# Optimization experiments

Measured on AMD Instinct MI355X. Metric: run time of the kernel, lower is better.

Reference implementation:

```python
import jax, jax.numpy as jnp
import numpy as np

ACT_BITS = 8
Q_B = 2 ** (ACT_BITS - 1)          # 128
EPS = 1e-6                          # module epsilon
GN_EPS = 1e-5                       # torch GroupNorm default eps
SCALE = 0.01                        # fixed ternary weight scale (buffer)
STRIDE = 1
PADDING = 1


def setup_inputs() -> dict:
    key = jax.random.key(0)
    k1, k2 = jax.random.split(key)
    x = jax.random.normal(k1, (16, 256, 64, 64), dtype=jnp.float32)
    weight = jax.random.normal(k2, (256, 256, 3, 3), dtype=jnp.float32)
    bias = jnp.zeros((256,), dtype=jnp.float32)
    ln_weight = jnp.ones((256,), dtype=jnp.float32)
    ln_bias = jnp.zeros((256,), dtype=jnp.float32)
    return {"x": x, "weight": weight, "bias": bias,
            "ln_weight": ln_weight, "ln_bias": ln_bias}


def _group_norm_1group(x, gamma, beta):
    # GroupNorm(1, C): normalize over (C, H, W) per sample, per-channel affine.
    mean = jnp.mean(x, axis=(1, 2, 3), keepdims=True)
    var = jnp.var(x, axis=(1, 2, 3), keepdims=True)
    xn = (x - mean) * jax.lax.rsqrt(var + GN_EPS)
    return xn * gamma[None, :, None, None] + beta[None, :, None, None]


def reference(x, weight, bias, ln_weight, ln_bias):
    # 1) GroupNorm
    x_ln = _group_norm_1group(x, ln_weight, ln_bias)

    # 2) BitNet absmax activation quantization (global absmax)
    gamma = jnp.maximum(jnp.max(jnp.abs(x_ln)), EPS)
    x_scaled = x_ln * (Q_B / gamma)
    x_clipped = jnp.clip(x_scaled, -Q_B + EPS, Q_B - EPS)
    x_quant = jnp.round(x_clipped)

    # 3) Ternary weight quantization with fixed scale: {-SCALE, 0, +SCALE}
    delta = 0.7 * jnp.mean(jnp.abs(weight))  # TTQ threshold
    w_q = jnp.where(weight > delta, SCALE,
                    jnp.where(weight < -delta, -SCALE, 0.0)).astype(weight.dtype)

    # 4) Conv2d (NCHW, OIHW)
    y = jax.lax.conv_general_dilated(
        x_quant, w_q,
        window_strides=(STRIDE, STRIDE),
        padding=[(PADDING, PADDING), (PADDING, PADDING)],
        dimension_numbers=("NCHW", "OIHW", "NCHW"),
        feature_group_count=1,
    )

    # 5) Dequant + bias
    y = y * (gamma / Q_B) + bias[None, :, None, None]
    return y
```

## Files before the change

### kernel.cpp

```cpp
#include <hip/hip_runtime.h>
#include <hip/hip_bf16.h>

#define CHW   1048576
#define XQ_BYTES 35684352u
#define WQ_OFF   35684352u
#define GNP_OFF  36864000u
#define CMM_OFF  36880384u
#define MR_OFF   36913152u
#define SC_OFF   36913280u
#define WP_OFF   36913296u
#define DL_OFF   36913584u

typedef __attribute__((ext_vector_type(8)))  short short8;
typedef __attribute__((ext_vector_type(16))) float f32x16;

__device__ __forceinline__ unsigned short f2bf(float f) {
    __hip_bfloat16 h = __float2bfloat16(f);
    return __builtin_bit_cast(unsigned short, h);
}

__device__ __forceinline__ void gload16(const void* g, void* l) {
    __builtin_amdgcn_global_load_lds(
        (const __attribute__((address_space(1))) unsigned int*)(unsigned long long)(g),
        (__attribute__((address_space(3))) unsigned int*)(unsigned int)(unsigned long long)(l),
        16, 0, 0);
}

__global__ void k_pass1(const float* __restrict__ x, double2* __restrict__ part,
                        float2* __restrict__ cmm) {
    int bid = blockIdx.x;
    int n = bid >> 6, c4 = bid & 63;
    int t = threadIdx.x, ch = t >> 6, lane = t & 63;
    int c = c4 * 4 + ch;
    const float4* p = (const float4*)(x + (size_t)n * CHW + (size_t)c * 4096);
    double s = 0.0, ss = 0.0;
    float mn = 1e30f, mx = -1e30f;
#pragma unroll
    for (int k = 0; k < 16; ++k) {
        float4 v = p[k * 64 + lane];
        mn = fminf(mn, fminf(fminf(v.x, v.y), fminf(v.z, v.w)));
        mx = fmaxf(mx, fmaxf(fmaxf(v.x, v.y), fmaxf(v.z, v.w)));
        double dx = v.x, dy = v.y, dz = v.z, dw = v.w;
        s  += dx + dy + dz + dw;
        ss += dx * dx + dy * dy + dz * dz + dw * dw;
    }
    for (int o = 32; o; o >>= 1) {
        s += __shfl_down(s, o); ss += __shfl_down(ss, o);
        mn = fminf(mn, __shfl_down(mn, o)); mx = fmaxf(mx, __shfl_down(mx, o));
    }
    __shared__ double sh0[4], sh1[4];
    if (lane == 0) {
        cmm[n * 256 + c] = make_float2(mn, mx);
        sh0[ch] = s; sh1[ch] = ss;
    }
    __syncthreads();
    if (t == 0)
        part[bid] = make_double2(sh0[0] + sh0[1] + sh0[2] + sh0[3],
                                 sh1[0] + sh1[1] + sh1[2] + sh1[3]);
}

__global__ void k_wsum(const float* __restrict__ w, double* __restrict__ wp) {
    int blk = blockIdx.x, t = threadIdx.x;
    const float4* p = (const float4*)(w + (size_t)blk * 16384);
    double s = 0.0;
#pragma unroll
    for (int j = 0; j < 16; ++j) {
        float4 v = p[j * 256 + t];
        s += fabs((double)v.x) + fabs((double)v.y) + fabs((double)v.z) + fabs((double)v.w);
    }
    for (int o = 32; o; o >>= 1) s += __shfl_down(s, o);
    __shared__ double sh[4];
    if ((t & 63) == 0) sh[t >> 6] = s;
    __syncthreads();
    if (t == 0) wp[blk] = sh[0] + sh[1] + sh[2] + sh[3];
}

__global__ void k_scalars(const double2* __restrict__ part, const float2* __restrict__ cmm,
                          const float* __restrict__ lnw, const float* __restrict__ lnb,
                          const double* __restrict__ wp,
                          float2* __restrict__ mr, float* __restrict__ sc,
                          float* __restrict__ dl) {
    __shared__ float shm[16], shr[16];
    int t = threadIdx.x;
    {
        int n = t >> 4, i = t & 15;
        double s = 0.0, ss = 0.0;
#pragma unroll
        for (int k = 0; k < 4; ++k) {
            double2 v = part[n * 64 + i * 4 + k];
            s += v.x; ss += v.y;
        }
        for (int o = 8; o; o >>= 1) { s += __shfl_down(s, o); ss += __shfl_down(ss, o); }
        if (i == 0) {
            double mean = s * (1.0 / 1048576.0);
            double var  = ss * (1.0 / 1048576.0) - mean * mean;
            shm[n] = (float)mean; shr[n] = (float)(1.0 / sqrt(var + 1e-5));
        }
    }
    __syncthreads();
    if (t < 16) mr[t] = make_float2(shm[t], shr[t]);
    float m = 0.0f;
#pragma unroll
    for (int k = 0; k < 16; ++k) {
        int idx = t + k * 256;
        int n = idx >> 8, c = idx & 255;
        float2 v = cmm[idx];
        float scale = lnw[c] * shr[n];
        float shift = lnb[c] - shm[n] * scale;
        m = fmaxf(m, fmaxf(fabsf(v.x * scale + shift), fabsf(v.y * scale + shift)));
    }
    for (int o = 32; o; o >>= 1) m = fmaxf(m, __shfl_down(m, o));
    __shared__ float shg[4];
    if ((t & 63) == 0) shg[t >> 6] = m;
    __syncthreads();
    if (t == 0) {
        float gamma = fmaxf(fmaxf(fmaxf(shg[0], shg[1]), fmaxf(shg[2], shg[3])), 1e-6f);
        sc[0] = gamma;
        sc[1] = 128.0f / gamma;
        sc[2] = (gamma / 128.0f) * 0.01f;
    }
    if (t < 64) {
        double s = (t < 36) ? wp[t] : 0.0;
        for (int o = 32; o; o >>= 1) s += __shfl_down(s, o);
        if (t == 0) dl[0] = (float)(0.7 * (s / 589824.0));
    }
}

__global__ void k_wquant(const float* __restrict__ w, const float* __restrict__ dl,
                         unsigned short* __restrict__ wq) {
    __shared__ float sw[2304];
    int co = blockIdx.x, t = threadIdx.x;
    const float* wr = w + (size_t)co * 2304;
#pragma unroll
    for (int j = 0; j < 9; ++j) sw[j * 256 + t] = wr[j * 256 + t];
    __syncthreads();
    float d = dl[0];
#pragma unroll
    for (int tap = 0; tap < 9; ++tap) {
        float v = sw[t * 9 + tap];
        float s = (v > d) ? 1.0f : ((v < -d) ? -1.0f : 0.0f);
        wq[tap * 65536 + co * 256 + t] = f2bf(s);
    }
}

__global__ void k_halo(unsigned short* __restrict__ xq) {
    int idx = blockIdx.x * 8 + (threadIdx.x >> 5);
    int n = idx / 260, p = idx - n * 260;
    int hh, ww;
    if (p < 66)       { hh = 0;        ww = p; }
    else if (p < 132) { hh = 65;       ww = p - 66; }
    else if (p < 196) { hh = p - 131;  ww = 0; }
    else              { hh = p - 195;  ww = 65; }
    uint4 z = make_uint4(0, 0, 0, 0);
    *(uint4*)(xq + ((size_t)(n * 66 + hh) * 66 + ww) * 256 + (threadIdx.x & 31) * 8) = z;
}

__global__ void k_quantx(const float* __restrict__ x, const float2* __restrict__ mr,
                         const float* __restrict__ sc, const float* __restrict__ lnw,
                         const float* __restrict__ lnb, unsigned short* __restrict__ xq) {
    int bid = blockIdx.x;
    int n = bid >> 6, hg = (bid >> 2) & 15, cg = bid & 3;
    int t = threadIdx.x;
    int w = t & 63, h = hg * 4 + (t >> 6);
    float2 m = mr[n];
    float s128 = sc[1];
    uint q[32];
    const float* xp = x + (((size_t)n * 256 + cg * 64) * 64 + h) * 64 + w;
#pragma unroll
    for (int ci = 0; ci < 64; ++ci) {
        int c = cg * 64 + ci;
        float g = lnw[c] * m.y;
        float be = lnb[c];
        float v = xp[(size_t)ci * 4096];
        float xs = ((v - m.x) * g + be) * s128;
        xs = fminf(fmaxf(xs, -(128.0f - 1e-6f)), (128.0f - 1e-6f));
        unsigned short ub = f2bf(rintf(xs));
        if (ci & 1) q[ci >> 1] |= ((uint)ub << 16);
        else        q[ci >> 1]  = ub;
    }
    unsigned short* op = xq + ((size_t)(n * 66 + h + 1) * 66 + (w + 1)) * 256 + cg * 64;
    uint4* o4 = (uint4*)op;
#pragma unroll
    for (int s2 = 0; s2 < 8; ++s2)
        o4[s2] = make_uint4(q[s2 * 4], q[s2 * 4 + 1], q[s2 * 4 + 2], q[s2 * 4 + 3]);
}

#define ATRI  16384
#define BBASE 49152
#define BBUF  16384

#define LD8(off) (*(const short8*)&lds[(off)])

#define STAGE_B(BS) { \
    const int _so = BBASE + (BS) * BBUF + dAB; \
    gload16(bSrc + stB,        &lds[_so]); \
    gload16(bSrc + stB + 2048, &lds[_so + 512]); \
    gload16(bSrc + stB + 4096, &lds[_so + 1024]); \
    gload16(bSrc + stB + 6144, &lds[_so + 1536]); \
    if (bKc < 3) { bKc++; stB += 64; } else { bKc = 0; stB += 65344; } }

#define STAGE_A(AS) { \
    const int _so = (AS) * ATRI + dAB; \
    gload16(aSrc + stA,        &lds[_so]); \
    gload16(aSrc + stA + 2048, &lds[_so + 512]); \
    gload16(aSrc + stA + 4096, &lds[_so + 1024]); \
    gload16(aSrc + stA + 6144, &lds[_so + 1536]); \
    if (aKc < 3) { aKc++; stA += 64; } \
    else { aKc = 0; if (aTx < 2) { aTx++; stA += 64; } else { aTx = 0; stA += 16192; } } }

#define ITER(AR, BR, AS, BS, DOA, DOB, W) { \
    const int _abo = (AR) * ATRI; \
    const int _bbo = BBASE + (BR) * BBUF; \
    if (DOB) STAGE_B(BS) \
    if (DOA) STAGE_A(AS) \
    short8 b00 = LD8(_bbo + rB0 + sp0), b01 = LD8(_bbo + rB0 + sp1); \
    short8 b02 = LD8(_bbo + rB0 + sp2), b03 = LD8(_bbo + rB0 + sp3); \
    short8 b10 = LD8(_bbo + rB1 + sp0), b11 = LD8(_bbo + rB1 + sp1); \
    short8 b12 = LD8(_bbo + rB1 + sp2), b13 = LD8(_bbo + rB1 + sp3); \
    _Pragma("unroll") \
    for (int _m = 0; _m < 4; ++_m) { \
        const int _ra = _abo + rA0 + _m * 2048; \
        short8 a0 = LD8(_ra + sp0), a1 = LD8(_ra + sp1); \
        short8 a2 = LD8(_ra + sp2), a3 = LD8(_ra + sp3); \
        __builtin_amdgcn_s_setprio(1); \
        acc[_m][0] = __builtin_amdgcn_mfma_f32_32x32x16_bf16(a0, b00, acc[_m][0], 0, 0, 0); \
        acc[_m][1] = __builtin_amdgcn_mfma_f32_32x32x16_bf16(a0, b10, acc[_m][1], 0, 0, 0); \
        acc[_m][0] = __builtin_amdgcn_mfma_f32_32x32x16_bf16(a1, b01, acc[_m][0], 0, 0, 0); \
        acc[_m][1] = __builtin_amdgcn_mfma_f32_32x32x16_bf16(a1, b11, acc[_m][1], 0, 0, 0); \
        acc[_m][0] = __builtin_amdgcn_mfma_f32_32x32x16_bf16(a2, b02, acc[_m][0], 0, 0, 0); \
        acc[_m][1] = __builtin_amdgcn_mfma_f32_32x32x16_bf16(a2, b12, acc[_m][1], 0, 0, 0); \
        acc[_m][0] = __builtin_amdgcn_mfma_f32_32x32x16_bf16(a3, b03, acc[_m][0], 0, 0, 0); \
        acc[_m][1] = __builtin_amdgcn_mfma_f32_32x32x16_bf16(a3, b13, acc[_m][1], 0, 0, 0); \
        __builtin_amdgcn_s_setprio(0); \
    } \
    if ((W) == 4)      { asm volatile("s_waitcnt vmcnt(4)" ::: "memory"); } \
    else if ((W) == 0) { asm volatile("s_waitcnt vmcnt(0)" ::: "memory"); } \
    __builtin_amdgcn_s_barrier(); \
    __builtin_amdgcn_sched_barrier(0); \
}

#define STORE4(P, A, BV) { \
    float4 v0; v0.x = (A)[0]*qs+(BV);  v0.y = (A)[1]*qs+(BV);  v0.z = (A)[2]*qs+(BV);  v0.w = (A)[3]*qs+(BV);  *(float4*)((P))      = v0; \
    float4 v1; v1.x = (A)[4]*qs+(BV);  v1.y = (A)[5]*qs+(BV);  v1.z = (A)[6]*qs+(BV);  v1.w = (A)[7]*qs+(BV);  *(float4*)((P) + 8)  = v1; \
    float4 v2; v2.x = (A)[8]*qs+(BV);  v2.y = (A)[9]*qs+(BV);  v2.z = (A)[10]*qs+(BV); v2.w = (A)[11]*qs+(BV); *(float4*)((P) + 16) = v2; \
    float4 v3; v3.x = (A)[12]*qs+(BV); v3.y = (A)[13]*qs+(BV); v3.z = (A)[14]*qs+(BV); v3.w = (A)[15]*qs+(BV); *(float4*)((P) + 24) = v3; }

__global__ __launch_bounds__(512, 2) void k_conv(const unsigned short* __restrict__ xq,
                                                 const unsigned short* __restrict__ wq,
                                                 const float* __restrict__ sc,
                                                 const float* __restrict__ bias,
                                                 float* __restrict__ out) {
    __shared__ unsigned short lds[81920];
    int t = threadIdx.x, wv = t >> 6, l = t & 63;
    int wm = wv >> 2, wn = wv & 3;
    int l31 = l & 31, l5 = l >> 5;

    int bid = ((int)blockIdx.x & 7) * 32 + ((int)blockIdx.x >> 3);
    int n = bid >> 4, h2 = (bid & 15) << 2;

    int rowg = l >> 3;
    int lg   = (l & 7) ^ rowg;
    const unsigned short* aSrc = xq +
        ((size_t)((n * 66 + h2 + (wv >> 1)) * 66 + (wv & 1) * 32 + rowg)) * 256 + lg * 8;
    const unsigned short* bSrc = wq + (size_t)(wv * 32 + rowg) * 256 + lg * 8;
    const int dAB = wv * 2048;

    int q7  = l31 & 7;
    int sp0 = ((0 + l5) ^ q7) * 8;
    int sp1 = ((2 + l5) ^ q7) * 8;
    int sp2 = ((4 + l5) ^ q7) * 8;
    int sp3 = ((6 + l5) ^ q7) * 8;
    int rA0 = (wm * 128 + l31) * 64;
    int rB0 = (wn * 64 + l31) * 64;
    int rB1 = rB0 + 2048;

    f32x16 acc[4][2] = {};

    gload16(aSrc,        &lds[dAB]);
    gload16(aSrc + 2048, &lds[dAB + 512]);
    gload16(aSrc + 4096, &lds[dAB + 1024]);
    gload16(aSrc + 6144, &lds[dAB + 1536]);
    gload16(bSrc,        &lds[BBASE + dAB]);
    gload16(bSrc + 2048, &lds[BBASE + dAB + 512]);
    gload16(bSrc + 4096, &lds[BBASE + dAB + 1024]);
    gload16(bSrc + 6144, &lds[BBASE + dAB + 1536]);
    gload16(aSrc + 64,        &lds[ATRI + dAB]);
    gload16(aSrc + 64 + 2048, &lds[ATRI + dAB + 512]);
    gload16(aSrc + 64 + 4096, &lds[ATRI + dAB + 1024]);
    gload16(aSrc + 64 + 6144, &lds[ATRI + dAB + 1536]);
    asm volatile("s_waitcnt vmcnt(4)" ::: "memory");
    __builtin_amdgcn_s_barrier();
    __builtin_amdgcn_sched_barrier(0);

    int stA = 128, aKc = 2, aTx = 0;
    int stB = 64,  bKc = 1;

#pragma unroll 1
    for (int it = 0; it < 5; ++it) {
        ITER(0, 0, 2, 1, 1, 1, 4)
        ITER(1, 1, 0, 0, 1, 1, 4)
        ITER(2, 0, 1, 1, 1, 1, 4)
        ITER(0, 1, 2, 0, 1, 1, 4)
        ITER(1, 0, 0, 1, 1, 1, 4)
        ITER(2, 1, 1, 0, 1, 1, 4)
    }
    ITER(0, 0, 2, 1, 1, 1, 4)
    ITER(1, 1, 0, 0, 1, 1, 4)
    ITER(2, 0, 1, 1, 1, 1, 4)
    ITER(0, 1, 2, 0, 1, 1, 4)
    ITER(1, 0, 0, 1, 0, 1, 0)
    ITER(2, 1, 0, 0, 0, 0, -1)

    float qs = sc[2];
#pragma unroll
    for (int m = 0; m < 4; ++m) {
        int h = h2 + wm * 2 + (m >> 1);
        int wb = (m & 1) * 32 + l5 * 4;
        size_t obase = (size_t)n * CHW + (size_t)h * 64 + wb;
#pragma unroll
        for (int nf = 0; nf < 2; ++nf) {
            int co = wn * 64 + nf * 32 + l31;
            float bv = bias[co];
            float* ob = out + obase + (size_t)co * 4096;
            STORE4(ob, acc[m][nf], bv)
        }
    }
}

extern "C" void kernel_launch(void* const* d_in, const int* in_sizes, int n_in,
                              void* d_out, int out_size, void* d_ws, size_t ws_size,
                              hipStream_t stream) {
    (void)in_sizes; (void)n_in; (void)out_size; (void)ws_size;
    const float* x    = (const float*)d_in[0];
    const float* wgt  = (const float*)d_in[1];
    const float* bias = (const float*)d_in[2];
    const float* lnw  = (const float*)d_in[3];
    const float* lnb  = (const float*)d_in[4];
    float* out = (float*)d_out;
    char* ws = (char*)d_ws;

    unsigned short* xq = (unsigned short*)ws;
    unsigned short* wq = (unsigned short*)(ws + WQ_OFF);
    double2* gnp = (double2*)(ws + GNP_OFF);
    float2*  cmm = (float2*)(ws + CMM_OFF);
    float2*  mr  = (float2*)(ws + MR_OFF);
    float*   sc  = (float*)(ws + SC_OFF);
    double*  wp  = (double*)(ws + WP_OFF);
    float*   dl  = (float*)(ws + DL_OFF);

    k_pass1  <<<1024, 256, 0, stream>>>(x, gnp, cmm);
    k_wsum   <<<36,   256, 0, stream>>>(wgt, wp);
    k_scalars<<<1,    256, 0, stream>>>(gnp, cmm, lnw, lnb, wp, mr, sc, dl);
    k_wquant <<<256,  256, 0, stream>>>(wgt, dl, wq);
    k_halo   <<<520,  256, 0, stream>>>(xq);
    k_quantx <<<1024, 256, 0, stream>>>(x, mr, sc, lnw, lnb, xq);
    k_conv   <<<256,  512, 0, stream>>>(xq, wq, sc, bias, out);
}
```

Before: 121.5 us.

## Switch conv to int8 MFMA with overflow-fixup pass for +128 activations

Quantized activations and ternary weights are stored as int8 instead of bf16, and the conv uses i32 32x32x32 int8 MFMA, which halves operand bytes and doubles K per instruction. Because +128 does not fit in int8, such values are clamped to 127 and recorded in an event list, and a separate fixup kernel atomically adds the missing contribution to the output. The quantx kernel is also re-tiled to a different thread and block mapping. The fixup path relies on a capped list of 1024 events and adds atomics and an extra launch.

```diff
diff --git a/kernel.cpp b/kernel.cpp
--- a/kernel.cpp
+++ b/kernel.cpp
@@ -2,22 +2,19 @@
 #include <hip/hip_bf16.h>
 
 #define CHW   1048576
-#define XQ_BYTES 35684352u
-#define WQ_OFF   35684352u
-#define GNP_OFF  36864000u
-#define CMM_OFF  36880384u
-#define MR_OFF   36913152u
-#define SC_OFF   36913280u
-#define WP_OFF   36913296u
-#define DL_OFF   36913584u
-
-typedef __attribute__((ext_vector_type(8)))  short short8;
-typedef __attribute__((ext_vector_type(16))) float f32x16;
-
-__device__ __forceinline__ unsigned short f2bf(float f) {
-    __hip_bfloat16 h = __float2bfloat16(f);
-    return __builtin_bit_cast(unsigned short, h);
-}
+#define XQ_BYTES 17842176u
+#define WQ_OFF   17842176u
+#define GNP_OFF  18432000u
+#define CMM_OFF  18448384u
+#define MR_OFF   18481152u
+#define SC_OFF   18481280u
+#define WP_OFF   18481296u
+#define DL_OFF   18481584u
+#define EVC_OFF  18481588u
+#define EVL_OFF  18481592u
+
+typedef __attribute__((ext_vector_type(4)))  int i32x4;
+typedef __attribute__((ext_vector_type(16))) int i32x16;
 
 __device__ __forceinline__ void gload16(const void* g, void* l) {
     __builtin_amdgcn_global_load_lds(
@@ -79,7 +76,7 @@
                           const float* __restrict__ lnw, const float* __restrict__ lnb,
                           const double* __restrict__ wp,
                           float2* __restrict__ mr, float* __restrict__ sc,
-                          float* __restrict__ dl) {
+                          float* __restrict__ dl, int* __restrict__ evcnt) {
     __shared__ float shm[16], shr[16];
     int t = threadIdx.x;
     {
@@ -99,6 +96,7 @@
     }
     __syncthreads();
     if (t < 16) mr[t] = make_float2(shm[t], shr[t]);
+    if (t == 0) evcnt[0] = 0;
     float m = 0.0f;
 #pragma unroll
     for (int k = 0; k < 16; ++k) {
@@ -127,7 +125,7 @@
 }
 
 __global__ void k_wquant(const float* __restrict__ w, const float* __restrict__ dl,
-                         unsigned short* __restrict__ wq) {
+                         signed char* __restrict__ wq) {
     __shared__ float sw[2304];
     int co = blockIdx.x, t = threadIdx.x;
     const float* wr = w + (size_t)co * 2304;
@@ -138,12 +136,12 @@
 #pragma unroll
     for (int tap = 0; tap < 9; ++tap) {
         float v = sw[t * 9 + tap];
-        float s = (v > d) ? 1.0f : ((v < -d) ? -1.0f : 0.0f);
-        wq[tap * 65536 + co * 256 + t] = f2bf(s);
-    }
-}
-
-__global__ void k_halo(unsigned short* __restrict__ xq) {
+        int s = (v > d) ? 1 : ((v < -d) ? -1 : 0);
+        wq[tap * 65536 + co * 256 + t] = (signed char)s;
+    }
+}
+
+__global__ void k_halo(unsigned char* __restrict__ xq) {
     int idx = blockIdx.x * 8 + (threadIdx.x >> 5);
     int n = idx / 260, p = idx - n * 260;
     int hh, ww;
@@ -151,106 +149,122 @@
     else if (p < 132) { hh = 65;       ww = p - 66; }
     else if (p < 196) { hh = p - 131;  ww = 0; }
     else              { hh = p - 195;  ww = 65; }
-    uint4 z = make_uint4(0, 0, 0, 0);
-    *(uint4*)(xq + ((size_t)(n * 66 + hh) * 66 + ww) * 256 + (threadIdx.x & 31) * 8) = z;
+    *(uint2*)(xq + ((size_t)(n * 66 + hh) * 66 + ww) * 256 + (threadIdx.x & 31) * 8) =
+        make_uint2(0, 0);
 }
 
 __global__ void k_quantx(const float* __restrict__ x, const float2* __restrict__ mr,
                          const float* __restrict__ sc, const float* __restrict__ lnw,
-                         const float* __restrict__ lnb, unsigned short* __restrict__ xq) {
+                         const float* __restrict__ lnb, unsigned char* __restrict__ xq,
+                         int* __restrict__ evcnt, int* __restrict__ evlist) {
     int bid = blockIdx.x;
-    int n = bid >> 6, hg = (bid >> 2) & 15, cg = bid & 3;
+    int n = bid >> 8, r = bid & 255;
+    int h = r >> 2, wg = r & 3;
     int t = threadIdx.x;
-    int w = t & 63, h = hg * 4 + (t >> 6);
+    int g = t & 15, p = t >> 4;
+    int w = wg * 16 + p;
     float2 m = mr[n];
     float s128 = sc[1];
-    uint q[32];
-    const float* xp = x + (((size_t)n * 256 + cg * 64) * 64 + h) * 64 + w;
-#pragma unroll
-    for (int ci = 0; ci < 64; ++ci) {
-        int c = cg * 64 + ci;
-        float g = lnw[c] * m.y;
-        float be = lnb[c];
-        float v = xp[(size_t)ci * 4096];
-        float xs = ((v - m.x) * g + be) * s128;
-        xs = fminf(fmaxf(xs, -(128.0f - 1e-6f)), (128.0f - 1e-6f));
-        unsigned short ub = f2bf(rintf(xs));
-        if (ci & 1) q[ci >> 1] |= ((uint)ub << 16);
-        else        q[ci >> 1]  = ub;
-    }
-    unsigned short* op = xq + ((size_t)(n * 66 + h + 1) * 66 + (w + 1)) * 256 + cg * 64;
-    uint4* o4 = (uint4*)op;
-#pragma unroll
-    for (int s2 = 0; s2 < 8; ++s2)
-        o4[s2] = make_uint4(q[s2 * 4], q[s2 * 4 + 1], q[s2 * 4 + 2], q[s2 * 4 + 3]);
-}
-
-#define ATRI  16384
+    const float* xp = x + ((size_t)n * 256 + g * 16) * 4096 + h * 64 + w;
+    uint u[4];
+#pragma unroll
+    for (int j = 0; j < 16; ++j) {
+        int c = g * 16 + j;
+        float gg = lnw[c] * m.y, be = lnb[c];
+        float v = xp[(size_t)j * 4096];
+        float xs = ((v - m.x) * gg + be) * s128;
+        xs = fminf(fmaxf(xs, -(128.0f - 1e-6f)), 128.0f - 1e-6f);
+        int q = (int)rintf(xs);
+        if (q == 128) {
+            int idx = atomicAdd(evcnt, 1);
+            if (idx < 1024) evlist[idx] = (n << 20) | (h << 14) | (w << 8) | c;
+            q = 127;
+        }
+        uint b = (uint)(q & 255);
+        if ((j & 3) == 0) u[j >> 2] = b; else u[j >> 2] |= b << ((j & 3) * 8);
+    }
+    *(uint4*)(xq + ((size_t)((n * 66 + h + 1) * 66) + (w + 1)) * 256 + g * 16) =
+        make_uint4(u[0], u[1], u[2], u[3]);
+}
+
+__global__ void k_fix(const signed char* __restrict__ wq, const int* __restrict__ evcnt,
+                      const int* __restrict__ evlist, const float* __restrict__ sc,
+                      float* __restrict__ out) {
+    int cnt = *evcnt; if (cnt > 1024) cnt = 1024;
+    float qs = sc[2];
+    int co = threadIdx.x;
+    for (int e = blockIdx.x; e < cnt; e += gridDim.x) {
+        int pk = evlist[e];
+        int n = pk >> 20, h = (pk >> 14) & 63, w = (pk >> 8) & 63, ci = pk & 255;
+#pragma unroll
+        for (int ty = 0; ty < 3; ++ty)
+#pragma unroll
+            for (int tx = 0; tx < 3; ++tx) {
+                int i = h + 1 - ty, j = w + 1 - tx;
+                if (i < 0 || i > 63 || j < 0 || j > 63) continue;
+                int sgn = wq[(ty * 3 + tx) * 65536 + co * 256 + ci];
+                if (sgn)
+                    atomicAdd(out + (((size_t)n * 256 + co) * 64 + i) * 64 + j,
+                              qs * (float)sgn);
+            }
+    }
+}
+
+#define ABUF  16384
 #define BBASE 49152
-#define BBUF  16384
-
-#define LD8(off) (*(const short8*)&lds[(off)])
-
-#define STAGE_B(BS) { \
-    const int _so = BBASE + (BS) * BBUF + dAB; \
-    gload16(bSrc + stB,        &lds[_so]); \
-    gload16(bSrc + stB + 2048, &lds[_so + 512]); \
-    gload16(bSrc + stB + 4096, &lds[_so + 1024]); \
-    gload16(bSrc + stB + 6144, &lds[_so + 1536]); \
-    if (bKc < 3) { bKc++; stB += 64; } else { bKc = 0; stB += 65344; } }
+#define LD16(off) (*(const i32x4*)&lds8[(off)])
+#define MFMA_I8(A, B, C) __builtin_amdgcn_mfma_i32_32x32x32_i8(A, B, C, 0, 0, 0)
 
 #define STAGE_A(AS) { \
-    const int _so = (AS) * ATRI + dAB; \
-    gload16(aSrc + stA,        &lds[_so]); \
-    gload16(aSrc + stA + 2048, &lds[_so + 512]); \
-    gload16(aSrc + stA + 4096, &lds[_so + 1024]); \
-    gload16(aSrc + stA + 6144, &lds[_so + 1536]); \
+    const int _so = (AS) * ABUF + wv * 1024; \
+    gload16(aSrc + stA,         lds8 + _so); \
+    gload16(aSrc + stA + 33792, lds8 + _so + 8192); \
     if (aKc < 3) { aKc++; stA += 64; } \
     else { aKc = 0; if (aTx < 2) { aTx++; stA += 64; } else { aTx = 0; stA += 16192; } } }
 
+#define STAGE_B(BS) { \
+    const int _so = BBASE + (BS) * ABUF + wv * 1024; \
+    gload16(bSrc + stB,         lds8 + _so); \
+    gload16(bSrc + stB + 32768, lds8 + _so + 8192); \
+    if (bKc < 3) { bKc++; stB += 64; } else { bKc = 0; stB += 65344; } }
+
 #define ITER(AR, BR, AS, BS, DOA, DOB, W) { \
-    const int _abo = (AR) * ATRI; \
-    const int _bbo = BBASE + (BR) * BBUF; \
+    const int _ab = (AR) * ABUF; \
+    const int _bb = BBASE + (BR) * ABUF; \
     if (DOB) STAGE_B(BS) \
     if (DOA) STAGE_A(AS) \
-    short8 b00 = LD8(_bbo + rB0 + sp0), b01 = LD8(_bbo + rB0 + sp1); \
-    short8 b02 = LD8(_bbo + rB0 + sp2), b03 = LD8(_bbo + rB0 + sp3); \
-    short8 b10 = LD8(_bbo + rB1 + sp0), b11 = LD8(_bbo + rB1 + sp1); \
-    short8 b12 = LD8(_bbo + rB1 + sp2), b13 = LD8(_bbo + rB1 + sp3); \
+    i32x4 b00 = LD16(_bb + rdB);          i32x4 b01 = LD16((_bb + rdB) ^ 32); \
+    i32x4 b10 = LD16(_bb + rdB + 2048);   i32x4 b11 = LD16((_bb + rdB + 2048) ^ 32); \
     _Pragma("unroll") \
     for (int _m = 0; _m < 4; ++_m) { \
-        const int _ra = _abo + rA0 + _m * 2048; \
-        short8 a0 = LD8(_ra + sp0), a1 = LD8(_ra + sp1); \
-        short8 a2 = LD8(_ra + sp2), a3 = LD8(_ra + sp3); \
+        const int _ra = _ab + rdA + _m * 2048; \
+        i32x4 a0 = LD16(_ra); \
+        i32x4 a1 = LD16(_ra ^ 32); \
         __builtin_amdgcn_s_setprio(1); \
-        acc[_m][0] = __builtin_amdgcn_mfma_f32_32x32x16_bf16(a0, b00, acc[_m][0], 0, 0, 0); \
-        acc[_m][1] = __builtin_amdgcn_mfma_f32_32x32x16_bf16(a0, b10, acc[_m][1], 0, 0, 0); \
-        acc[_m][0] = __builtin_amdgcn_mfma_f32_32x32x16_bf16(a1, b01, acc[_m][0], 0, 0, 0); \
-        acc[_m][1] = __builtin_amdgcn_mfma_f32_32x32x16_bf16(a1, b11, acc[_m][1], 0, 0, 0); \
-        acc[_m][0] = __builtin_amdgcn_mfma_f32_32x32x16_bf16(a2, b02, acc[_m][0], 0, 0, 0); \
-        acc[_m][1] = __builtin_amdgcn_mfma_f32_32x32x16_bf16(a2, b12, acc[_m][1], 0, 0, 0); \
-        acc[_m][0] = __builtin_amdgcn_mfma_f32_32x32x16_bf16(a3, b03, acc[_m][0], 0, 0, 0); \
-        acc[_m][1] = __builtin_amdgcn_mfma_f32_32x32x16_bf16(a3, b13, acc[_m][1], 0, 0, 0); \
+        acc[_m][0] = MFMA_I8(a0, b00, acc[_m][0]); \
+        acc[_m][1] = MFMA_I8(a0, b10, acc[_m][1]); \
+        acc[_m][0] = MFMA_I8(a1, b01, acc[_m][0]); \
+        acc[_m][1] = MFMA_I8(a1, b11, acc[_m][1]); \
         __builtin_amdgcn_s_setprio(0); \
     } \
-    if ((W) == 4)      { asm volatile("s_waitcnt vmcnt(4)" ::: "memory"); } \
+    if ((W) == 2)      { asm volatile("s_waitcnt vmcnt(2)" ::: "memory"); } \
     else if ((W) == 0) { asm volatile("s_waitcnt vmcnt(0)" ::: "memory"); } \
     __builtin_amdgcn_s_barrier(); \
     __builtin_amdgcn_sched_barrier(0); \
 }
 
 #define STORE4(P, A, BV) { \
-    float4 v0; v0.x = (A)[0]*qs+(BV);  v0.y = (A)[1]*qs+(BV);  v0.z = (A)[2]*qs+(BV);  v0.w = (A)[3]*qs+(BV);  *(float4*)((P))      = v0; \
-    float4 v1; v1.x = (A)[4]*qs+(BV);  v1.y = (A)[5]*qs+(BV);  v1.z = (A)[6]*qs+(BV);  v1.w = (A)[7]*qs+(BV);  *(float4*)((P) + 8)  = v1; \
-    float4 v2; v2.x = (A)[8]*qs+(BV);  v2.y = (A)[9]*qs+(BV);  v2.z = (A)[10]*qs+(BV); v2.w = (A)[11]*qs+(BV); *(float4*)((P) + 16) = v2; \
-    float4 v3; v3.x = (A)[12]*qs+(BV); v3.y = (A)[13]*qs+(BV); v3.z = (A)[14]*qs+(BV); v3.w = (A)[15]*qs+(BV); *(float4*)((P) + 24) = v3; }
-
-__global__ __launch_bounds__(512, 2) void k_conv(const unsigned short* __restrict__ xq,
-                                                 const unsigned short* __restrict__ wq,
+    float4 v0; v0.x = (float)(A)[0]*qs+(BV);  v0.y = (float)(A)[1]*qs+(BV);  v0.z = (float)(A)[2]*qs+(BV);  v0.w = (float)(A)[3]*qs+(BV);  *(float4*)((P))      = v0; \
+    float4 v1; v1.x = (float)(A)[4]*qs+(BV);  v1.y = (float)(A)[5]*qs+(BV);  v1.z = (float)(A)[6]*qs+(BV);  v1.w = (float)(A)[7]*qs+(BV);  *(float4*)((P) + 8)  = v1; \
+    float4 v2; v2.x = (float)(A)[8]*qs+(BV);  v2.y = (float)(A)[9]*qs+(BV);  v2.z = (float)(A)[10]*qs+(BV); v2.w = (float)(A)[11]*qs+(BV); *(float4*)((P) + 16) = v2; \
+    float4 v3; v3.x = (float)(A)[12]*qs+(BV); v3.y = (float)(A)[13]*qs+(BV); v3.z = (float)(A)[14]*qs+(BV); v3.w = (float)(A)[15]*qs+(BV); *(float4*)((P) + 24) = v3; }
+
+__global__ __launch_bounds__(512, 2) void k_conv(const unsigned char* __restrict__ xq,
+                                                 const signed char* __restrict__ wq,
                                                  const float* __restrict__ sc,
                                                  const float* __restrict__ bias,
                                                  float* __restrict__ out) {
-    __shared__ unsigned short lds[81920];
+    __shared__ __align__(128) unsigned char lds8[81920];
     int t = threadIdx.x, wv = t >> 6, l = t & 63;
     int wm = wv >> 2, wn = wv & 3;
     int l31 = l & 31, l5 = l >> 5;
@@ -258,56 +272,46 @@
     int bid = ((int)blockIdx.x & 7) * 32 + ((int)blockIdx.x >> 3);
     int n = bid >> 4, h2 = (bid & 15) << 2;
 
-    int rowg = l >> 3;
-    int lg   = (l & 7) ^ rowg;
-    const unsigned short* aSrc = xq +
-        ((size_t)((n * 66 + h2 + (wv >> 1)) * 66 + (wv & 1) * 32 + rowg)) * 256 + lg * 8;
-    const unsigned short* bSrc = wq + (size_t)(wv * 32 + rowg) * 256 + lg * 8;
-    const int dAB = wv * 2048;
-
-    int q7  = l31 & 7;
-    int sp0 = ((0 + l5) ^ q7) * 8;
-    int sp1 = ((2 + l5) ^ q7) * 8;
-    int sp2 = ((4 + l5) ^ q7) * 8;
-    int sp3 = ((6 + l5) ^ q7) * 8;
-    int rA0 = (wm * 128 + l31) * 64;
-    int rB0 = (wn * 64 + l31) * 64;
-    int rB1 = rB0 + 2048;
-
-    f32x16 acc[4][2] = {};
-
-    gload16(aSrc,        &lds[dAB]);
-    gload16(aSrc + 2048, &lds[dAB + 512]);
-    gload16(aSrc + 4096, &lds[dAB + 1024]);
-    gload16(aSrc + 6144, &lds[dAB + 1536]);
-    gload16(bSrc,        &lds[BBASE + dAB]);
-    gload16(bSrc + 2048, &lds[BBASE + dAB + 512]);
-    gload16(bSrc + 4096, &lds[BBASE + dAB + 1024]);
-    gload16(bSrc + 6144, &lds[BBASE + dAB + 1536]);
-    gload16(aSrc + 64,        &lds[ATRI + dAB]);
-    gload16(aSrc + 64 + 2048, &lds[ATRI + dAB + 512]);
-    gload16(aSrc + 64 + 4096, &lds[ATRI + dAB + 1024]);
-    gload16(aSrc + 64 + 6144, &lds[ATRI + dAB + 1536]);
-    asm volatile("s_waitcnt vmcnt(4)" ::: "memory");
+    int s_src = (l & 7) ^ (l >> 3);
+    int sb2   = (s_src >> 2) & 1;
+    int skc   = s_src & 3;
+    int RA    = wv * 16 + ((l >> 3) << 1) + sb2;
+    int hsub  = RA >> 6, wA = RA & 63;
+    const unsigned char* aSrc = xq +
+        ((size_t)(n * 66 + h2 + hsub) * 66 + wA) * 256 + skc * 16;
+    int coB = ((wv * 8 + (l >> 3)) << 1) + sb2;
+    const unsigned char* bSrc = (const unsigned char*)wq + (size_t)coB * 256 + skc * 16;
+
+    int q3    = (l31 >> 1) & 7;
+    int s0    = ((l31 & 1) << 2) | l5;
+    int phys0 = s0 ^ q3;
+    int rdA = (wm * 64 + (l31 >> 1)) * 128 + phys0 * 16;
+    int rdB = (wn * 32 + (l31 >> 1)) * 128 + phys0 * 16;
+
+    i32x16 acc[4][2] = {};
+
+    int stA = 0, aKc = 0, aTx = 0;
+    int stB = 0, bKc = 0;
+    STAGE_A(0)
+    STAGE_B(0)
+    STAGE_A(1)
+    asm volatile("s_waitcnt vmcnt(2)" ::: "memory");
     __builtin_amdgcn_s_barrier();
     __builtin_amdgcn_sched_barrier(0);
 
-    int stA = 128, aKc = 2, aTx = 0;
-    int stB = 64,  bKc = 1;
-
 #pragma unroll 1
     for (int it = 0; it < 5; ++it) {
-        ITER(0, 0, 2, 1, 1, 1, 4)
-        ITER(1, 1, 0, 0, 1, 1, 4)
-        ITER(2, 0, 1, 1, 1, 1, 4)
-        ITER(0, 1, 2, 0, 1, 1, 4)
-        ITER(1, 0, 0, 1, 1, 1, 4)
-        ITER(2, 1, 1, 0, 1, 1, 4)
-    }
-    ITER(0, 0, 2, 1, 1, 1, 4)
-    ITER(1, 1, 0, 0, 1, 1, 4)
-    ITER(2, 0, 1, 1, 1, 1, 4)
-    ITER(0, 1, 2, 0, 1, 1, 4)
+        ITER(0, 0, 2, 1, 1, 1, 2)
+        ITER(1, 1, 0, 0, 1, 1, 2)
+        ITER(2, 0, 1, 1, 1, 1, 2)
+        ITER(0, 1, 2, 0, 1, 1, 2)
+        ITER(1, 0, 0, 1, 1, 1, 2)
+        ITER(2, 1, 1, 0, 1, 1, 2)
+    }
+    ITER(0, 0, 2, 1, 1, 1, 2)
+    ITER(1, 1, 0, 0, 1, 1, 2)
+    ITER(2, 0, 1, 1, 1, 1, 2)
+    ITER(0, 1, 2, 0, 1, 1, 2)
     ITER(1, 0, 0, 1, 0, 1, 0)
     ITER(2, 1, 0, 0, 0, 0, -1)
 
@@ -339,20 +343,23 @@
     float* out = (float*)d_out;
     char* ws = (char*)d_ws;
 
-    unsigned short* xq = (unsigned short*)ws;
-    unsigned short* wq = (unsigned short*)(ws + WQ_OFF);
+    unsigned char* xq  = (unsigned char*)ws;
+    signed char*   wq  = (signed char*)(ws + WQ_OFF);
     double2* gnp = (double2*)(ws + GNP_OFF);
     float2*  cmm = (float2*)(ws + CMM_OFF);
     float2*  mr  = (float2*)(ws + MR_OFF);
     float*   sc  = (float*)(ws + SC_OFF);
     double*  wp  = (double*)(ws + WP_OFF);
     float*   dl  = (float*)(ws + DL_OFF);
+    int*     evc = (int*)(ws + EVC_OFF);
+    int*     evl = (int*)(ws + EVL_OFF);
 
     k_pass1  <<<1024, 256, 0, stream>>>(x, gnp, cmm);
     k_wsum   <<<36,   256, 0, stream>>>(wgt, wp);
-    k_scalars<<<1,    256, 0, stream>>>(gnp, cmm, lnw, lnb, wp, mr, sc, dl);
+    k_scalars<<<1,    256, 0, stream>>>(gnp, cmm, lnw, lnb, wp, mr, sc, dl, evc);
     k_wquant <<<256,  256, 0, stream>>>(wgt, dl, wq);
     k_halo   <<<520,  256, 0, stream>>>(xq);
-    k_quantx <<<1024, 256, 0, stream>>>(x, mr, sc, lnw, lnb, xq);
+    k_quantx <<<4096, 256, 0, stream>>>(x, mr, sc, lnw, lnb, xq, evc, evl);
     k_conv   <<<256,  512, 0, stream>>>(xq, wq, sc, bias, out);
-}
+    k_fix    <<<64,   256, 0, stream>>>(wq, evc, evl, sc, out);
+}
```

After: 166.1 us. 1.37x slower.
